# Kernel tuning notes

Hardware: AMD Instinct MI355X
Metric: run time of the kernel (lower is better)

## Reference

```python
import jax, jax.numpy as jnp
import numpy as np

N_NODES = 50000


def _spmm(edge_index, edge_vals, dense):
    """Sparse [N,N] @ dense [N,D] via gather + segment-sum.
    edge_index[0] = row (dst), edge_index[1] = col (src)."""
    dst, src = edge_index[0], edge_index[1]
    msgs = edge_vals[:, None] * dense[src]  # [E, D]
    return jax.ops.segment_sum(msgs, dst, num_segments=N_NODES)


def setup_inputs() -> dict:
    key = jax.random.key(0)
    ks = jax.random.split(key, 8)
    N, D_IN, D_OUT, E = N_NODES, 128, 128, 800000
    x = jax.random.normal(ks[0], (N, D_IN), dtype=jnp.float32)
    # glorot init for weights
    scale = jnp.sqrt(6.0 / (D_IN + D_OUT)).astype(jnp.float32)
    W0 = jax.random.uniform(ks[1], (D_IN, D_OUT), jnp.float32, -scale, scale)
    W1 = jax.random.uniform(ks[2], (D_IN, D_OUT), jnp.float32, -scale, scale)
    bias = jnp.zeros((D_OUT,), dtype=jnp.float32)
    edge_vals0 = jax.random.uniform(ks[3], (E,), dtype=jnp.float32)
    edge_vals1 = jax.random.uniform(ks[4], (E,), dtype=jnp.float32)
    edge_index0 = jax.random.randint(ks[5], (2, E), 0, N, dtype=jnp.int32)
    edge_index1 = jax.random.randint(ks[6], (2, E), 0, N, dtype=jnp.int32)
    return {"x": x, "W0": W0, "W1": W1, "bias": bias,
            "edge_vals0": edge_vals0, "edge_vals1": edge_vals1,
            "edge_index0": edge_index0, "edge_index1": edge_index1}


def reference(x, W0, W1, bias, edge_vals0, edge_vals1, edge_index0, edge_index1):
    # dropout with rate 0 == identity (self.dropout unset in source snippet)
    pre0 = x @ W0  # [N, D_out]
    pre1 = x @ W1
    out = _spmm(edge_index0, edge_vals0, pre0) + _spmm(edge_index1, edge_vals1, pre1)
    out = out + bias
    return jax.nn.relu(out)
```

## Files before the change

### kernel.cpp

```cpp
#include <hip/hip_runtime.h>
#include <hip/hip_bf16.h>


#define BROWS 32
#define NBUCK 1563
#define NB2 2048
#define BCAP 704
#define ACAP (2 * BCAP)
#define FT5 8192
#define PREROWS 65536

typedef __attribute__((ext_vector_type(8))) short bf16x8;
typedef __attribute__((ext_vector_type(4))) float f32x4;

__device__ inline unsigned short f2bf(float f) {
    union { float f; unsigned u; } v; v.f = f;
    unsigned r = v.u + 0x7fff + ((v.u >> 16) & 1);
    return (unsigned short)(r >> 16);
}

__global__ __launch_bounds__(256) void prep_kernel(
    const float* __restrict__ W0, const float* __restrict__ W1,
    unsigned short* __restrict__ wt0, unsigned short* __restrict__ wt1,
    int* __restrict__ cur, int ncur)
{
    const int bid = blockIdx.x;
    const int tid = threadIdx.x;
    if (bid >= 8) {
        for (int i = tid; i < ncur; i += 256) cur[i] = 0;
        return;
    }
    const int which = bid >> 2;
    const int k0 = (bid & 3) * 32;
    const float* __restrict__ W = which ? W1 : W0;
    unsigned short* __restrict__ wt = which ? wt1 : wt0;
    for (int i = tid; i < 32 * 128; i += 256) {
        int k = k0 + (i >> 7), n = i & 127;
        wt[n * 128 + k] = f2bf(W[k * 128 + n]);
    }
}

__global__ __launch_bounds__(512) void gemm_fused_kernel(
    const float* __restrict__ x,
    const unsigned short* __restrict__ wt0,
    const unsigned short* __restrict__ wt1,
    unsigned short* __restrict__ pre,
    int N)
{
    __shared__ unsigned short sA[16][136];
    __shared__ short ctile[8][16][40];

    const int tid = threadIdx.x;
    const int m0 = blockIdx.x * 16;

    {
        int r = tid >> 5;
        int c4 = (tid & 31) << 2;
        float4 v = *(const float4*)&x[(m0 + r) * 128 + c4];
        ushort4 s;
        s.x = f2bf(v.x); s.y = f2bf(v.y); s.z = f2bf(v.z); s.w = f2bf(v.w);
        *(ushort4*)&sA[r][c4] = s;
    }
    __syncthreads();

    const int w = tid >> 6;
    const int lane = tid & 63;
    const int adj = w >> 2;
    const int wq = w & 3;
    const unsigned short* __restrict__ wt = adj ? wt1 : wt0;
    unsigned short* __restrict__ po = pre + (size_t)adj * PREROWS * 128;
    const int l15 = lane & 15;
    const int quad = lane >> 4;
    const int nA = wq * 32 + l15;

    f32x4 c0 = {0.f, 0.f, 0.f, 0.f};
    f32x4 c1 = {0.f, 0.f, 0.f, 0.f};
#pragma unroll
    for (int k0 = 0; k0 < 128; k0 += 32) {
        union { bf16x8 v; ushort4 h[2]; } au;
        au.h[0] = *(const ushort4*)&sA[l15][k0 + quad * 8];
        au.h[1] = *(const ushort4*)&sA[l15][k0 + quad * 8 + 4];
        bf16x8 b0 = *(const bf16x8*)&wt[nA * 128 + k0 + quad * 8];
        bf16x8 b1 = *(const bf16x8*)&wt[(nA + 16) * 128 + k0 + quad * 8];
        c0 = __builtin_amdgcn_mfma_f32_16x16x32_bf16(au.v, b0, c0, 0, 0, 0);
        c1 = __builtin_amdgcn_mfma_f32_16x16x32_bf16(au.v, b1, c1, 0, 0, 0);
    }

#pragma unroll
    for (int i = 0; i < 4; ++i) {
        ctile[w][quad * 4 + i][l15]      = (short)f2bf(c0[i]);
        ctile[w][quad * 4 + i][16 + l15] = (short)f2bf(c1[i]);
    }
    const int rr = lane >> 2, cg = (lane & 3) * 8;
    ushort4 s0 = *(ushort4*)&ctile[w][rr][cg];
    ushort4 s1 = *(ushort4*)&ctile[w][rr][cg + 4];
    int row = m0 + rr;
    *(ushort4*)&po[row * 128 + wq * 32 + cg] = s0;
    *(ushort4*)&po[row * 128 + wq * 32 + cg + 4] = s1;
}

__global__ __launch_bounds__(1024) void fill5_kernel(
    const int* __restrict__ ei0, const int* __restrict__ ei1,
    const float* __restrict__ ev0, const float* __restrict__ ev1,
    int* __restrict__ cur, int2* __restrict__ recs, int E)
{
    __shared__ int2 srt[FT5];
    __shared__ unsigned short skey[FT5];
    __shared__ int lcnt[NB2];
    __shared__ int bstart[NB2];
    __shared__ int lcur[NB2];
    __shared__ int gpos[NBUCK];
    __shared__ int glim[NBUCK];
    __shared__ int part[1024];

    const int a = blockIdx.y;
    const int* __restrict__ ei = a ? ei1 : ei0;
    const float* __restrict__ ev = a ? ev1 : ev0;
    const int tid = threadIdx.x;
    const int e0 = blockIdx.x * FT5;

    lcnt[tid] = 0; lcnt[tid + 1024] = 0;
    __syncthreads();

    int2 rec[8];
    int key8[8];
#pragma unroll
    for (int j = 0; j < 8; ++j) {
        int e = e0 + j * 1024 + tid;
        if (e < E) {
            int d = ei[e];
            int s = ei[E + e];
            key8[j] = d >> 5;
            rec[j] = make_int2(((d & 31) << 17) | (a << 16) | s,
                               __float_as_int(ev[e]));
            atomicAdd(&lcnt[key8[j]], 1);
        } else key8[j] = -1;
    }
    __syncthreads();

    int c0 = lcnt[2 * tid], c1 = lcnt[2 * tid + 1];
    int tsum = c0 + c1;
    part[tid] = tsum;
    __syncthreads();
    for (int o = 1; o < 1024; o <<= 1) {
        int t = (tid >= o) ? part[tid - o] : 0;
        __syncthreads();
        part[tid] += t;
        __syncthreads();
    }
    int run = part[tid] - tsum;
    const int total = part[1023];
    bstart[2 * tid] = run; lcur[2 * tid] = run;
    bstart[2 * tid + 1] = run + c0; lcur[2 * tid + 1] = run + c0;

#pragma unroll
    for (int h = 0; h < 2; ++h) {
        int k = 2 * tid + h;
        int c = h ? c1 : c0;
        if (k < NBUCK && c > 0) {
            int bin = k * 2 + a;
            int g = atomicAdd(&cur[bin], c);
            int lim = BCAP - g; if (lim < 0) lim = 0;
            gpos[k] = bin * BCAP + g;
            glim[k] = lim;
        }
    }
    __syncthreads();

#pragma unroll
    for (int j = 0; j < 8; ++j) {
        if (key8[j] >= 0) {
            int p = atomicAdd(&lcur[key8[j]], 1);
            srt[p] = rec[j];
            skey[p] = (unsigned short)key8[j];
        }
    }
    __syncthreads();

    for (int i = tid; i < total; i += 1024) {
        int k = skey[i];
        int r = i - bstart[k];
        if (r < glim[k]) recs[gpos[k] + r] = srt[i];
    }
}

__global__ __launch_bounds__(256, 6) void aggregate9_kernel(
    const int* __restrict__ cur, const int2* __restrict__ recs,
    const unsigned short* __restrict__ pre,
    const float* __restrict__ bias,
    float* __restrict__ out, int N)
{
    __shared__ int2 srec[ACAP];
    __shared__ int2 srt[ACAP];
    __shared__ int lcnt[32];
    __shared__ int lstart[32];
    __shared__ int lcur[32];

    const int b = blockIdx.x;
    const int tid = threadIdx.x;

    int n0 = cur[2 * b];     if (n0 > BCAP) n0 = BCAP;
    int n1 = cur[2 * b + 1]; if (n1 > BCAP) n1 = BCAP;
    const int total = n0 + n1;
    const int base0 = (2 * b) * BCAP, base1 = (2 * b + 1) * BCAP;

    if (tid < 32) lcnt[tid] = 0;
    __syncthreads();

    for (int i = tid; i < total; i += 256) {
        int2 r = (i < n0) ? recs[base0 + i] : recs[base1 + i - n0];
        srec[i] = r;
        atomicAdd(&lcnt[(r.x >> 17) & 31], 1);
    }
    __syncthreads();

    if (tid < 32) {
        int cme = lcnt[tid];
        int p = cme;
#pragma unroll
        for (int o = 1; o < 32; o <<= 1) {
            int t = __shfl_up(p, o);
            if (tid >= o) p += t;
        }
        lstart[tid] = p - cme;
        lcur[tid] = p - cme;
    }
    __syncthreads();

    for (int i = tid; i < total; i += 256) {
        int2 r = srec[i];
        srt[atomicAdd(&lcur[(r.x >> 17) & 31], 1)] = r;
    }
    __syncthreads();

    const int wv = tid >> 6;
    const int lane = tid & 63;
    const float2 bi = *(const float2*)&bias[lane * 2];

#define GA(r) (*(const unsigned*)&pre[((r).x & 0x1ffff) * 128 + 2 * lane])
#define ACC(r, u) { float v = __int_as_float((r).y);                    \
        acc.x = fmaf(v, __uint_as_float((u) << 16), acc.x);             \
        acc.y = fmaf(v, __uint_as_float((u) & 0xffff0000u), acc.y); }

    for (int t = 0; t < 8; ++t) {
        const int rl = wv * 8 + t;
        const int s = lstart[rl];
        const int e = s + lcnt[rl];
        float2 acc = make_float2(0.f, 0.f);
        int j = s;
        for (; j + 8 <= e; j += 8) {
            int2 r0 = srt[j], r1 = srt[j + 1], r2 = srt[j + 2], r3 = srt[j + 3];
            int2 r4 = srt[j + 4], r5 = srt[j + 5], r6 = srt[j + 6], r7 = srt[j + 7];
            unsigned u0 = GA(r0), u1 = GA(r1), u2 = GA(r2), u3 = GA(r3);
            unsigned u4 = GA(r4), u5 = GA(r5), u6 = GA(r6), u7 = GA(r7);
            ACC(r0, u0); ACC(r1, u1); ACC(r2, u2); ACC(r3, u3);
            ACC(r4, u4); ACC(r5, u5); ACC(r6, u6); ACC(r7, u7);
        }
        for (; j + 4 <= e; j += 4) {
            int2 r0 = srt[j], r1 = srt[j + 1], r2 = srt[j + 2], r3 = srt[j + 3];
            unsigned u0 = GA(r0), u1 = GA(r1), u2 = GA(r2), u3 = GA(r3);
            ACC(r0, u0); ACC(r1, u1); ACC(r2, u2); ACC(r3, u3);
        }
        for (; j < e; ++j) {
            int2 r0 = srt[j];
            unsigned u0 = GA(r0);
            ACC(r0, u0);
        }
        int row = b * BROWS + rl;
        if (row < N) {
            float2 o;
            o.x = fmaxf(acc.x + bi.x, 0.f);
            o.y = fmaxf(acc.y + bi.y, 0.f);
            *(float2*)&out[row * 128 + 2 * lane] = o;
        }
    }
#undef GA
#undef ACC
}

extern "C" void kernel_launch(void* const* d_in, const int* in_sizes, int n_in,
                              void* d_out, int out_size, void* d_ws, size_t ws_size,
                              hipStream_t stream) {
    const float* x    = (const float*)d_in[0];
    const float* W0   = (const float*)d_in[1];
    const float* W1   = (const float*)d_in[2];
    const float* bias = (const float*)d_in[3];
    const float* ev0  = (const float*)d_in[4];
    const float* ev1  = (const float*)d_in[5];
    const int*   ei0  = (const int*)d_in[6];
    const int*   ei1  = (const int*)d_in[7];
    float* out = (float*)d_out;

    const int N = in_sizes[0] / 128;
    const int E = in_sizes[4];
    const int NBINS2 = NBUCK * 2;

    char* w = (char*)d_ws;
    unsigned short* pre = (unsigned short*)w;   w += (size_t)2 * PREROWS * 128 * 2;
    unsigned short* wt0 = (unsigned short*)w;   w += (size_t)128 * 128 * 2;
    unsigned short* wt1 = (unsigned short*)w;   w += (size_t)128 * 128 * 2;
    int* cur = (int*)w;                         w += (size_t)NBINS2 * 4;
    int2* recs = (int2*)w;                      w += (size_t)NBINS2 * BCAP * 8;

    prep_kernel<<<9, 256, 0, stream>>>(W0, W1, wt0, wt1, cur, NBINS2);

    gemm_fused_kernel<<<N / 16, 512, 0, stream>>>(x, wt0, wt1, pre, N);

    dim3 fgrid((E + FT5 - 1) / FT5, 2);
    fill5_kernel<<<fgrid, 1024, 0, stream>>>(ei0, ei1, ev0, ev1, cur, recs, E);

    aggregate9_kernel<<<NBUCK, 256, 0, stream>>>(cur, recs, pre, bias, out, N);
}
```

Baseline: 203.4 us.

## Merge GEMM and edge bucketing into one launch with smaller fill tiles

Combines the bf16 MFMA projection GEMM and the edge bucket-fill pass into a single kernel. Block indices below nfill do bucketing and the rest do GEMM rows, with shared memory overlaid through a union. The fill tile drops to 4096 edges with 512 threads, uses vectorized int4/float4 edge loads, and replaces the block-wide barrier scan with a wave-shuffle scan. The aim is to overlap the compute-bound GEMM with the atomic-heavy fill and remove one launch gap. In exchange, the larger union shared-memory footprint may lower occupancy for the GEMM blocks.

```diff
diff --git a/kernel.cpp b/kernel.cpp
--- a/kernel.cpp
+++ b/kernel.cpp
@@ -7,7 +7,7 @@
 #define NB2 2048
 #define BCAP 704
 #define ACAP (2 * BCAP)
-#define FT5 8192
+#define FT6 4096
 #define PREROWS 65536
 
 typedef __attribute__((ext_vector_type(8))) short bf16x8;
@@ -40,147 +40,178 @@
     }
 }
 
-__global__ __launch_bounds__(512) void gemm_fused_kernel(
+struct FillSM {
+    int2 srt[FT6];
+    alignas(16) int lcnt[NB2];
+    alignas(16) int lcur[NB2];
+    unsigned short skey[FT6];
+    int gpos[NBUCK];
+    int glim[NBUCK];
+    int wsum[8];
+    int total;
+};
+struct GemmSM {
+    unsigned short sA[16][136];
+    short ctile[8][16][40];
+};
+union MidSM { FillSM f; GemmSM g; };
+
+__global__ __launch_bounds__(512) void mid_kernel(
     const float* __restrict__ x,
     const unsigned short* __restrict__ wt0,
     const unsigned short* __restrict__ wt1,
     unsigned short* __restrict__ pre,
-    int N)
-{
-    __shared__ unsigned short sA[16][136];
-    __shared__ short ctile[8][16][40];
-
-    const int tid = threadIdx.x;
-    const int m0 = blockIdx.x * 16;
-
-    {
-        int r = tid >> 5;
-        int c4 = (tid & 31) << 2;
-        float4 v = *(const float4*)&x[(m0 + r) * 128 + c4];
-        ushort4 s;
-        s.x = f2bf(v.x); s.y = f2bf(v.y); s.z = f2bf(v.z); s.w = f2bf(v.w);
-        *(ushort4*)&sA[r][c4] = s;
-    }
-    __syncthreads();
-
-    const int w = tid >> 6;
-    const int lane = tid & 63;
-    const int adj = w >> 2;
-    const int wq = w & 3;
-    const unsigned short* __restrict__ wt = adj ? wt1 : wt0;
-    unsigned short* __restrict__ po = pre + (size_t)adj * PREROWS * 128;
-    const int l15 = lane & 15;
-    const int quad = lane >> 4;
-    const int nA = wq * 32 + l15;
-
-    f32x4 c0 = {0.f, 0.f, 0.f, 0.f};
-    f32x4 c1 = {0.f, 0.f, 0.f, 0.f};
-#pragma unroll
-    for (int k0 = 0; k0 < 128; k0 += 32) {
-        union { bf16x8 v; ushort4 h[2]; } au;
-        au.h[0] = *(const ushort4*)&sA[l15][k0 + quad * 8];
-        au.h[1] = *(const ushort4*)&sA[l15][k0 + quad * 8 + 4];
-        bf16x8 b0 = *(const bf16x8*)&wt[nA * 128 + k0 + quad * 8];
-        bf16x8 b1 = *(const bf16x8*)&wt[(nA + 16) * 128 + k0 + quad * 8];
-        c0 = __builtin_amdgcn_mfma_f32_16x16x32_bf16(au.v, b0, c0, 0, 0, 0);
-        c1 = __builtin_amdgcn_mfma_f32_16x16x32_bf16(au.v, b1, c1, 0, 0, 0);
-    }
-
-#pragma unroll
-    for (int i = 0; i < 4; ++i) {
-        ctile[w][quad * 4 + i][l15]      = (short)f2bf(c0[i]);
-        ctile[w][quad * 4 + i][16 + l15] = (short)f2bf(c1[i]);
-    }
-    const int rr = lane >> 2, cg = (lane & 3) * 8;
-    ushort4 s0 = *(ushort4*)&ctile[w][rr][cg];
-    ushort4 s1 = *(ushort4*)&ctile[w][rr][cg + 4];
-    int row = m0 + rr;
-    *(ushort4*)&po[row * 128 + wq * 32 + cg] = s0;
-    *(ushort4*)&po[row * 128 + wq * 32 + cg + 4] = s1;
-}
-
-__global__ __launch_bounds__(1024) void fill5_kernel(
     const int* __restrict__ ei0, const int* __restrict__ ei1,
     const float* __restrict__ ev0, const float* __restrict__ ev1,
-    int* __restrict__ cur, int2* __restrict__ recs, int E)
+    int* __restrict__ cur, int2* __restrict__ recs,
+    int E, int N, int nfill)
 {
-    __shared__ int2 srt[FT5];
-    __shared__ unsigned short skey[FT5];
-    __shared__ int lcnt[NB2];
-    __shared__ int bstart[NB2];
-    __shared__ int lcur[NB2];
-    __shared__ int gpos[NBUCK];
-    __shared__ int glim[NBUCK];
-    __shared__ int part[1024];
-
-    const int a = blockIdx.y;
-    const int* __restrict__ ei = a ? ei1 : ei0;
-    const float* __restrict__ ev = a ? ev1 : ev0;
+    __shared__ MidSM sm;
     const int tid = threadIdx.x;
-    const int e0 = blockIdx.x * FT5;
-
-    lcnt[tid] = 0; lcnt[tid + 1024] = 0;
-    __syncthreads();
-
-    int2 rec[8];
-    int key8[8];
-#pragma unroll
-    for (int j = 0; j < 8; ++j) {
-        int e = e0 + j * 1024 + tid;
-        if (e < E) {
-            int d = ei[e];
-            int s = ei[E + e];
-            key8[j] = d >> 5;
-            rec[j] = make_int2(((d & 31) << 17) | (a << 16) | s,
-                               __float_as_int(ev[e]));
-            atomicAdd(&lcnt[key8[j]], 1);
-        } else key8[j] = -1;
-    }
-    __syncthreads();
-
-    int c0 = lcnt[2 * tid], c1 = lcnt[2 * tid + 1];
-    int tsum = c0 + c1;
-    part[tid] = tsum;
-    __syncthreads();
-    for (int o = 1; o < 1024; o <<= 1) {
-        int t = (tid >= o) ? part[tid - o] : 0;
-        __syncthreads();
-        part[tid] += t;
-        __syncthreads();
-    }
-    int run = part[tid] - tsum;
-    const int total = part[1023];
-    bstart[2 * tid] = run; lcur[2 * tid] = run;
-    bstart[2 * tid + 1] = run + c0; lcur[2 * tid + 1] = run + c0;
-
-#pragma unroll
-    for (int h = 0; h < 2; ++h) {
-        int k = 2 * tid + h;
-        int c = h ? c1 : c0;
-        if (k < NBUCK && c > 0) {
-            int bin = k * 2 + a;
-            int g = atomicAdd(&cur[bin], c);
-            int lim = BCAP - g; if (lim < 0) lim = 0;
-            gpos[k] = bin * BCAP + g;
-            glim[k] = lim;
-        }
-    }
-    __syncthreads();
-
-#pragma unroll
-    for (int j = 0; j < 8; ++j) {
-        if (key8[j] >= 0) {
-            int p = atomicAdd(&lcur[key8[j]], 1);
-            srt[p] = rec[j];
-            skey[p] = (unsigned short)key8[j];
-        }
-    }
-    __syncthreads();
-
-    for (int i = tid; i < total; i += 1024) {
-        int k = skey[i];
-        int r = i - bstart[k];
-        if (r < glim[k]) recs[gpos[k] + r] = srt[i];
+    const int bx = blockIdx.x;
+
+    if (bx < nfill) {
+        FillSM& F = sm.f;
+        const int a = bx & 1;
+        const int e0 = (bx >> 1) * FT6;
+        const int* __restrict__ ei = a ? ei1 : ei0;
+        const float* __restrict__ ev = a ? ev1 : ev0;
+
+        ((int4*)F.lcnt)[tid] = make_int4(0, 0, 0, 0);
+        __syncthreads();
+
+        const int eb = e0 + tid * 8;
+        int dd[8], ss[8]; float vv[8];
+        if (e0 + FT6 <= E) {
+            int4 d0 = *(const int4*)(ei + eb);
+            int4 d1 = *(const int4*)(ei + eb + 4);
+            int4 s0 = *(const int4*)(ei + E + eb);
+            int4 s1 = *(const int4*)(ei + E + eb + 4);
+            float4 v0 = *(const float4*)(ev + eb);
+            float4 v1 = *(const float4*)(ev + eb + 4);
+            dd[0] = d0.x; dd[1] = d0.y; dd[2] = d0.z; dd[3] = d0.w;
+            dd[4] = d1.x; dd[5] = d1.y; dd[6] = d1.z; dd[7] = d1.w;
+            ss[0] = s0.x; ss[1] = s0.y; ss[2] = s0.z; ss[3] = s0.w;
+            ss[4] = s1.x; ss[5] = s1.y; ss[6] = s1.z; ss[7] = s1.w;
+            vv[0] = v0.x; vv[1] = v0.y; vv[2] = v0.z; vv[3] = v0.w;
+            vv[4] = v1.x; vv[5] = v1.y; vv[6] = v1.z; vv[7] = v1.w;
+        } else {
+#pragma unroll
+            for (int j = 0; j < 8; ++j) {
+                int e = eb + j;
+                if (e < E) { dd[j] = ei[e]; ss[j] = ei[E + e]; vv[j] = ev[e]; }
+            }
+        }
+        int key8[8]; int2 rec[8];
+#pragma unroll
+        for (int j = 0; j < 8; ++j) {
+            if (eb + j < E) {
+                key8[j] = dd[j] >> 5;
+                rec[j] = make_int2(((dd[j] & 31) << 17) | (a << 16) | ss[j],
+                                   __float_as_int(vv[j]));
+                atomicAdd(&F.lcnt[key8[j]], 1);
+            } else key8[j] = -1;
+        }
+        __syncthreads();
+
+        const int lane = tid & 63;
+        const int wv = tid >> 6;
+        int4 c4 = ((const int4*)F.lcnt)[tid];
+        int cc[4] = { c4.x, c4.y, c4.z, c4.w };
+        int tsum = cc[0] + cc[1] + cc[2] + cc[3];
+        int p = tsum;
+#pragma unroll
+        for (int o = 1; o < 64; o <<= 1) {
+            int t = __shfl_up(p, o);
+            if (lane >= o) p += t;
+        }
+        if (lane == 63) F.wsum[wv] = p;
+        __syncthreads();
+        int wbase = 0;
+#pragma unroll
+        for (int w2 = 0; w2 < 7; ++w2) wbase += (w2 < wv) ? F.wsum[w2] : 0;
+        if (tid == 511) F.total = wbase + p;
+        int off = wbase + p - tsum;
+        const int k0 = 4 * tid;
+#pragma unroll
+        for (int h = 0; h < 4; ++h) {
+            F.lcur[k0 + h] = off;
+            if (k0 + h < NBUCK && cc[h] > 0) {
+                int bin = (k0 + h) * 2 + a;
+                int g = atomicAdd(&cur[bin], cc[h]);
+                int lim = BCAP - g; if (lim < 0) lim = 0;
+                F.gpos[k0 + h] = bin * BCAP + g;
+                F.glim[k0 + h] = lim;
+            }
+            off += cc[h];
+        }
+        __syncthreads();
+
+#pragma unroll
+        for (int j = 0; j < 8; ++j) {
+            if (key8[j] >= 0) {
+                int pp = atomicAdd(&F.lcur[key8[j]], 1);
+                F.srt[pp] = rec[j];
+                F.skey[pp] = (unsigned short)key8[j];
+            }
+        }
+        __syncthreads();
+
+        const int total = F.total;
+        for (int i = tid; i < total; i += 512) {
+            int k = F.skey[i];
+            int st = k ? F.lcur[k - 1] : 0;
+            int r = i - st;
+            if (r < F.glim[k]) recs[F.gpos[k] + r] = F.srt[i];
+        }
+    } else {
+        GemmSM& G = sm.g;
+        const int m0 = (bx - nfill) * 16;
+
+        {
+            int r = tid >> 5;
+            int c4i = (tid & 31) << 2;
+            float4 v = *(const float4*)&x[(m0 + r) * 128 + c4i];
+            ushort4 s;
+            s.x = f2bf(v.x); s.y = f2bf(v.y); s.z = f2bf(v.z); s.w = f2bf(v.w);
+            *(ushort4*)&G.sA[r][c4i] = s;
+        }
+        __syncthreads();
+
+        const int w = tid >> 6;
+        const int lane = tid & 63;
+        const int adj = w >> 2;
+        const int wq = w & 3;
+        const unsigned short* __restrict__ wt = adj ? wt1 : wt0;
+        unsigned short* __restrict__ po = pre + (size_t)adj * PREROWS * 128;
+        const int l15 = lane & 15;
+        const int quad = lane >> 4;
+        const int nA = wq * 32 + l15;
+
+        f32x4 c0 = {0.f, 0.f, 0.f, 0.f};
+        f32x4 c1 = {0.f, 0.f, 0.f, 0.f};
+#pragma unroll
+        for (int k0 = 0; k0 < 128; k0 += 32) {
+            union { bf16x8 v; ushort4 h[2]; } au;
+            au.h[0] = *(const ushort4*)&G.sA[l15][k0 + quad * 8];
+            au.h[1] = *(const ushort4*)&G.sA[l15][k0 + quad * 8 + 4];
+            bf16x8 b0 = *(const bf16x8*)&wt[nA * 128 + k0 + quad * 8];
+            bf16x8 b1 = *(const bf16x8*)&wt[(nA + 16) * 128 + k0 + quad * 8];
+            c0 = __builtin_amdgcn_mfma_f32_16x16x32_bf16(au.v, b0, c0, 0, 0, 0);
+            c1 = __builtin_amdgcn_mfma_f32_16x16x32_bf16(au.v, b1, c1, 0, 0, 0);
+        }
+
+#pragma unroll
+        for (int i = 0; i < 4; ++i) {
+            G.ctile[w][quad * 4 + i][l15]      = (short)f2bf(c0[i]);
+            G.ctile[w][quad * 4 + i][16 + l15] = (short)f2bf(c1[i]);
+        }
+        const int rr = lane >> 2, cg = (lane & 3) * 8;
+        ushort4 s0 = *(ushort4*)&G.ctile[w][rr][cg];
+        ushort4 s1 = *(ushort4*)&G.ctile[w][rr][cg + 4];
+        int row = m0 + rr;
+        *(ushort4*)&po[row * 128 + wq * 32 + cg] = s0;
+        *(ushort4*)&po[row * 128 + wq * 32 + cg + 4] = s1;
     }
 }
 
@@ -304,10 +335,10 @@
 
     prep_kernel<<<9, 256, 0, stream>>>(W0, W1, wt0, wt1, cur, NBINS2);
 
-    gemm_fused_kernel<<<N / 16, 512, 0, stream>>>(x, wt0, wt1, pre, N);
-
-    dim3 fgrid((E + FT5 - 1) / FT5, 2);
-    fill5_kernel<<<fgrid, 1024, 0, stream>>>(ei0, ei1, ev0, ev1, cur, recs, E);
+    const int nfill = 2 * ((E + FT6 - 1) / FT6);
+    const int ngemm = N / 16;
+    mid_kernel<<<nfill + ngemm, 512, 0, stream>>>(
+        x, wt0, wt1, pre, ei0, ei1, ev0, ev1, cur, recs, E, N, nfill);
 
     aggregate9_kernel<<<NBUCK, 256, 0, stream>>>(cur, recs, pre, bias, out, N);
 }
```

After: 220.3 us. +8.3%, slower.
